# Kernel optimization log

Hardware: AMD Instinct MI355X
Metric: run time of the kernel (lower is better)

## Reference

```python
import jax, jax.numpy as jnp
import numpy as np

Np_, Ny, Nu = 5, 8, 4
NZ = Np_ * (Ny + Nu)  # 60


def setup_inputs() -> dict:
    key = jax.random.key(0)
    ks = jax.random.split(key, 6)
    B, T = 8192, 1024
    u = jax.random.normal(ks[0], (B, T, Nu), dtype=jnp.float32)
    z0 = jax.random.normal(ks[1], (B, NZ), dtype=jnp.float32)
    W1 = jax.random.normal(ks[2], (NZ, 128), dtype=jnp.float32) * (1.0 / np.sqrt(NZ))
    b1 = jnp.zeros((128,), dtype=jnp.float32)
    W2 = jax.random.normal(ks[3], (128, 128), dtype=jnp.float32) * (1.0 / np.sqrt(128))
    b2 = jnp.zeros((128,), dtype=jnp.float32)
    W3 = jax.random.normal(ks[4], (128, Ny), dtype=jnp.float32) * (1.0 / np.sqrt(128))
    b3 = jnp.zeros((Ny,), dtype=jnp.float32)
    return {"u": u, "z0": z0, "W1": W1, "b1": b1, "W2": W2, "b2": b2,
            "W3": W3, "b3": b3}


def reference(u, z0, W1, b1, W2, b2, W3, b3):
    # u: [B, T, Nu], z0: [B, Np*(Ny+Nu)] -> y sequence [B, T, Ny]
    def step(z, u_t):
        h = jnp.tanh(z @ W1 + b1)
        h = jnp.tanh(h @ W2 + b2)
        y = h @ W3 + b3                      # [B, Ny]
        ypseq = z[:, : Np_ * Ny]
        upseq = z[:, Np_ * Ny:]
        z_new = jnp.concatenate(
            (ypseq[:, Ny:], y, upseq[:, Nu:], u_t), axis=-1)
        return z_new, y

    u_tbc = jnp.transpose(u, (1, 0, 2))      # [T, B, Nu]
    _, ys = jax.lax.scan(step, z0, u_tbc)    # ys: [T, B, Ny]
    return jnp.transpose(ys, (1, 0, 2))      # [B, T, Ny]
```

## Files before the change

### kernel.cpp

```cpp
#include <hip/hip_runtime.h>

#define T_STEPS 1024
#define NZV 60
#define H 128
#define NY 8
#define NU 4
#define ZSTR 72
#define HSTR 136

typedef __attribute__((ext_vector_type(8))) short bf16x8;
typedef __attribute__((ext_vector_type(4))) short bf16x4;
typedef __attribute__((ext_vector_type(4))) float f32x4;

__device__ __forceinline__ unsigned short f2bf(float x) {
    unsigned u = __float_as_uint(x);
    u += 0x7FFFu + ((u >> 16) & 1u);
    return (unsigned short)(u >> 16);
}

__device__ __forceinline__ unsigned cvt_pk_bf16(float lo, float hi) {
    unsigned r;
    asm("v_cvt_pk_bf16_f32 %0, %1, %2" : "=v"(r) : "v"(lo), "v"(hi));
    return r;
}

__device__ __forceinline__ float tanh_fast(float x) {
    float e = __builtin_amdgcn_exp2f(x * 2.8853900817779268f);
    return fmaf(-2.0f, __builtin_amdgcn_rcpf(e + 1.0f), 1.0f);
}

__global__ __launch_bounds__(256, 2)
void cstr_scan_kernel(const float* __restrict__ u_g, const float* __restrict__ z0_g,
                      const float* __restrict__ W1, const float* __restrict__ b1,
                      const float* __restrict__ W2, const float* __restrict__ b2,
                      const float* __restrict__ W3, const float* __restrict__ b3,
                      float* __restrict__ out) {
    __shared__ unsigned short zbuf[2][16][ZSTR];
    __shared__ unsigned short h1s[16][HSTR];
    __shared__ unsigned short h2s[16][HSTR];
    __shared__ float ybuf[16][16][NY];

    const int tid   = threadIdx.x;
    const int wid   = tid >> 6;
    const int lane  = tid & 63;
    const int b0    = blockIdx.x * 16;
    const int col   = lane & 15;
    const int kg    = lane >> 4;
    const int wrow0 = kg * 4;
    const int urow  = lane >> 2;
    const int uc    = lane & 3;
    const int nbase = wid * 32;

    bf16x8 w1f[2][2], w2f[4][2], w3f[4];
    float b1v[2], b2v[2], b3v;
#pragma unroll
    for (int nl = 0; nl < 2; ++nl) {
        b1v[nl] = b1[nbase + nl * 16 + col];
        b2v[nl] = b2[nbase + nl * 16 + col];
    }
    b3v = (col < NY) ? b3[col] : 0.f;

#pragma unroll
    for (int kc = 0; kc < 2; ++kc)
#pragma unroll
        for (int nl = 0; nl < 2; ++nl) {
            bf16x8 v;
#pragma unroll
            for (int j = 0; j < 8; ++j) {
                int k = kc * 32 + kg * 8 + j;
                float w = (k < NZV) ? W1[k * H + nbase + nl * 16 + col] : 0.f;
                v[j] = (short)f2bf(w);
            }
            w1f[kc][nl] = v;
        }
#pragma unroll
    for (int kc = 0; kc < 4; ++kc)
#pragma unroll
        for (int nl = 0; nl < 2; ++nl) {
            bf16x8 v;
#pragma unroll
            for (int j = 0; j < 8; ++j) {
                int k = kc * 32 + kg * 8 + j;
                v[j] = (short)f2bf(W2[k * H + nbase + nl * 16 + col]);
            }
            w2f[kc][nl] = v;
        }
#pragma unroll
    for (int kc = 0; kc < 4; ++kc) {
        bf16x8 v;
#pragma unroll
        for (int j = 0; j < 8; ++j) {
            int k = kc * 32 + kg * 8 + j;
            float w = (col < NY) ? W3[k * NY + col] : 0.f;
            v[j] = (short)f2bf(w);
        }
        w3f[kc] = v;
    }

    {
        unsigned short* zs = &zbuf[0][0][0];
        for (int i = tid; i < 2 * 16 * ZSTR; i += 256) zs[i] = 0;
        __syncthreads();
        for (int i = tid; i < 16 * NZV; i += 256) {
            int r = i / NZV, c = i - r * NZV;
            zbuf[0][r][c] = f2bf(z0_g[(size_t)(b0 + r) * NZV + c]);
        }
        __syncthreads();
    }

    const float* uptr = u_g + (size_t)(b0 + urow) * (T_STEPS * NU) + uc;
    float ureg = 0.f, ureg_n = 0.f;
    if (wid == 3) ureg = *uptr;

    int t = 0;

#define STEP_BODY(CUR)                                                                  \
    {                                                                                   \
        const int nxt = (CUR) ^ 1;                                                      \
                                    \
        bf16x8 za0 = *(const bf16x8*)&zbuf[CUR][col][kg * 8];                           \
        bf16x8 za1 = *(const bf16x8*)&zbuf[CUR][col][32 + kg * 8];                      \
        _Pragma("unroll")                                                               \
        for (int nl = 0; nl < 2; ++nl) {                                                \
            f32x4 c1 = { b1v[nl], b1v[nl], b1v[nl], b1v[nl] };                          \
            c1 = __builtin_amdgcn_mfma_f32_16x16x32_bf16(za0, w1f[0][nl], c1, 0, 0, 0); \
            c1 = __builtin_amdgcn_mfma_f32_16x16x32_bf16(za1, w1f[1][nl], c1, 0, 0, 0); \
            unsigned p01 = cvt_pk_bf16(tanh_fast(c1[0]), tanh_fast(c1[1]));             \
            unsigned p23 = cvt_pk_bf16(tanh_fast(c1[2]), tanh_fast(c1[3]));             \
            const int n = nbase + nl * 16 + col;                                        \
            h1s[wrow0 + 0][n] = (unsigned short)p01;                                    \
            h1s[wrow0 + 1][n] = (unsigned short)(p01 >> 16);                            \
            h1s[wrow0 + 2][n] = (unsigned short)p23;                                    \
            h1s[wrow0 + 3][n] = (unsigned short)(p23 >> 16);                            \
        }                                                                               \
                \
        if (wid == 3) {                                                                 \
            bf16x4 m0 = *(const bf16x4*)&zbuf[CUR][urow][8 + 8 * uc];                   \
            bf16x4 m1 = *(const bf16x4*)&zbuf[CUR][urow][12 + 8 * uc];                  \
            bf16x4 m2 = *(const bf16x4*)&zbuf[CUR][urow][44 + 4 * uc];                  \
            *(bf16x4*)&zbuf[nxt][urow][8 * uc]      = m0;                               \
            *(bf16x4*)&zbuf[nxt][urow][8 * uc + 4]  = m1;                               \
            *(bf16x4*)&zbuf[nxt][urow][40 + 4 * uc] = m2;                               \
            zbuf[nxt][urow][56 + uc] = f2bf(ureg);                                      \
            uptr += NU;                                                                 \
            if (t + 1 < T_STEPS) ureg_n = *uptr;                                        \
        }                                                                               \
        __syncthreads();                      \
                                              \
        bf16x8 ha0 = *(const bf16x8*)&h1s[col][0 * 32 + kg * 8];                        \
        bf16x8 ha1 = *(const bf16x8*)&h1s[col][1 * 32 + kg * 8];                        \
        bf16x8 ha2 = *(const bf16x8*)&h1s[col][2 * 32 + kg * 8];                        \
        bf16x8 ha3 = *(const bf16x8*)&h1s[col][3 * 32 + kg * 8];                        \
        _Pragma("unroll")                                                               \
        for (int nl = 0; nl < 2; ++nl) {                                                \
            f32x4 a0 = { b2v[nl], b2v[nl], b2v[nl], b2v[nl] };                          \
            f32x4 a1 = { 0.f, 0.f, 0.f, 0.f };                                          \
            a0 = __builtin_amdgcn_mfma_f32_16x16x32_bf16(ha0, w2f[0][nl], a0, 0, 0, 0); \
            a1 = __builtin_amdgcn_mfma_f32_16x16x32_bf16(ha1, w2f[1][nl], a1, 0, 0, 0); \
            a0 = __builtin_amdgcn_mfma_f32_16x16x32_bf16(ha2, w2f[2][nl], a0, 0, 0, 0); \
            a1 = __builtin_amdgcn_mfma_f32_16x16x32_bf16(ha3, w2f[3][nl], a1, 0, 0, 0); \
            f32x4 c2 = a0 + a1;                                                         \
            unsigned p01 = cvt_pk_bf16(tanh_fast(c2[0]), tanh_fast(c2[1]));             \
            unsigned p23 = cvt_pk_bf16(tanh_fast(c2[2]), tanh_fast(c2[3]));             \
            const int n = nbase + nl * 16 + col;                                        \
            h2s[wrow0 + 0][n] = (unsigned short)p01;                                    \
            h2s[wrow0 + 1][n] = (unsigned short)(p01 >> 16);                            \
            h2s[wrow0 + 2][n] = (unsigned short)p23;                                    \
            h2s[wrow0 + 3][n] = (unsigned short)(p23 >> 16);                            \
        }                                                                               \
        __syncthreads();                                              \
                              \
        if (wid == 0) {                                                                 \
            bf16x8 hp0 = *(const bf16x8*)&h2s[col][0 * 32 + kg * 8];                    \
            bf16x8 hp1 = *(const bf16x8*)&h2s[col][1 * 32 + kg * 8];                    \
            bf16x8 hp2 = *(const bf16x8*)&h2s[col][2 * 32 + kg * 8];                    \
            bf16x8 hp3 = *(const bf16x8*)&h2s[col][3 * 32 + kg * 8];                    \
            f32x4 ya = { b3v, b3v, b3v, b3v };                                          \
            f32x4 yb = { 0.f, 0.f, 0.f, 0.f };                                          \
            ya = __builtin_amdgcn_mfma_f32_16x16x32_bf16(hp0, w3f[0], ya, 0, 0, 0);     \
            yb = __builtin_amdgcn_mfma_f32_16x16x32_bf16(hp1, w3f[1], yb, 0, 0, 0);     \
            ya = __builtin_amdgcn_mfma_f32_16x16x32_bf16(hp2, w3f[2], ya, 0, 0, 0);     \
            yb = __builtin_amdgcn_mfma_f32_16x16x32_bf16(hp3, w3f[3], yb, 0, 0, 0);     \
            f32x4 y = ya + yb;                                                          \
            if (col < NY) {                                                             \
                unsigned q01 = cvt_pk_bf16(y[0], y[1]);                                 \
                unsigned q23 = cvt_pk_bf16(y[2], y[3]);                                 \
                zbuf[nxt][wrow0 + 0][32 + col] = (unsigned short)q01;                   \
                zbuf[nxt][wrow0 + 1][32 + col] = (unsigned short)(q01 >> 16);           \
                zbuf[nxt][wrow0 + 2][32 + col] = (unsigned short)q23;                   \
                zbuf[nxt][wrow0 + 3][32 + col] = (unsigned short)(q23 >> 16);           \
                const int ts = t & 15;                                                  \
                ybuf[ts][wrow0 + 0][col] = y[0];                                        \
                ybuf[ts][wrow0 + 1][col] = y[1];                                        \
                ybuf[ts][wrow0 + 2][col] = y[2];                                        \
                ybuf[ts][wrow0 + 3][col] = y[3];                                        \
            }                                                                           \
        }                                                                               \
        __syncthreads();               \
        ureg = ureg_n;                                                                  \
        ++t;                                                                            \
    }

    const int frow  = tid >> 4;
    const int ftoff = tid & 15;

#define FLUSH(BASE_T)                                                                   \
    {                                                                                   \
        const f32x4* yp = (const f32x4*)&ybuf[ftoff][frow][0];                          \
        f32x4 v0 = yp[0], v1 = yp[1];                                                   \
        float* op = out + ((size_t)(b0 + frow) * T_STEPS + (BASE_T) + ftoff) * NY;      \
        *(f32x4*)op = v0;                                                               \
        *(f32x4*)(op + 4) = v1;                                                         \
    }

#pragma unroll 1
    for (int it = 0; it < T_STEPS / 2; ++it) {
        if ((t & 15) == 0 && t > 0)
            FLUSH(t - 16);
        STEP_BODY(0)
        STEP_BODY(1)
    }
    FLUSH(T_STEPS - 16);
#undef STEP_BODY
#undef FLUSH
}

extern "C" void kernel_launch(void* const* d_in, const int* in_sizes, int n_in,
                              void* d_out, int out_size, void* d_ws, size_t ws_size,
                              hipStream_t stream) {
    (void)in_sizes; (void)n_in; (void)d_ws; (void)ws_size; (void)out_size;
    const float* u  = (const float*)d_in[0];
    const float* z0 = (const float*)d_in[1];
    const float* W1 = (const float*)d_in[2];
    const float* b1 = (const float*)d_in[3];
    const float* W2 = (const float*)d_in[4];
    const float* b2 = (const float*)d_in[5];
    const float* W3 = (const float*)d_in[6];
    const float* b3 = (const float*)d_in[7];
    float* out = (float*)d_out;

    dim3 grid(8192 / 16);
    dim3 block(256);
    cstr_scan_kernel<<<grid, block, 0, stream>>>(u, z0, W1, b1, W2, b2, W3, b3, out);
}
```

Before: 1.083 ms.

## Fuse layer-3 output into next step's layer-1 to drop a barrier per step

Every wave now redundantly computes the small W3 output (with transposed operands) at the start of the next step. The fresh y values are fed straight into the layer-1 A operand through a lane shuffle instead of waiting for a shared-memory round trip. This removes the third __syncthreads per timestep and the serialized single-wave layer-3 phase, at the cost of extra MFMAs on all four waves. The change also double-buffers h2s and ybuf to avoid races, and adds a prologue and epilogue for the pipeline.

```diff
diff --git a/kernel.cpp b/kernel.cpp
--- a/kernel.cpp
+++ b/kernel.cpp
@@ -12,6 +12,8 @@
 typedef __attribute__((ext_vector_type(4))) short bf16x4;
 typedef __attribute__((ext_vector_type(4))) float f32x4;
 
+union U4 { unsigned u[4]; bf16x8 v; };
+
 __device__ __forceinline__ unsigned short f2bf(float x) {
     unsigned u = __float_as_uint(x);
     u += 0x7FFFu + ((u >> 16) & 1u);
@@ -28,6 +30,8 @@
     float e = __builtin_amdgcn_exp2f(x * 2.8853900817779268f);
     return fmaf(-2.0f, __builtin_amdgcn_rcpf(e + 1.0f), 1.0f);
 }
+
+#define MFMA __builtin_amdgcn_mfma_f32_16x16x32_bf16
 
 __global__ __launch_bounds__(256, 2)
 void cstr_scan_kernel(const float* __restrict__ u_g, const float* __restrict__ z0_g,
@@ -37,8 +41,8 @@
                       float* __restrict__ out) {
     __shared__ unsigned short zbuf[2][16][ZSTR];
     __shared__ unsigned short h1s[16][HSTR];
-    __shared__ unsigned short h2s[16][HSTR];
-    __shared__ float ybuf[16][16][NY];
+    __shared__ unsigned short h2s[2][16][HSTR];
+    __shared__ float ybuf[32][16][NY];
 
     const int tid   = threadIdx.x;
     const int wid   = tid >> 6;
@@ -50,16 +54,22 @@
     const int urow  = lane >> 2;
     const int uc    = lane & 3;
     const int nbase = wid * 32;
-
-    bf16x8 w1f[2][2], w2f[4][2], w3f[4];
-    float b1v[2], b2v[2], b3v;
+    const int frow  = tid >> 4;
+    const int ftoff = tid & 15;
+
+    bf16x8 w1f[2][2], w2f[4][2], w3tf[4];
+    float b1v[2], b2v[2];
+    f32x4 b3t;
 #pragma unroll
     for (int nl = 0; nl < 2; ++nl) {
         b1v[nl] = b1[nbase + nl * 16 + col];
         b2v[nl] = b2[nbase + nl * 16 + col];
     }
-    b3v = (col < NY) ? b3[col] : 0.f;
-
+#pragma unroll
+    for (int r = 0; r < 4; ++r) {
+        int m = kg * 4 + r;
+        b3t[r] = (m < NY) ? b3[m] : 0.f;
+    }
 #pragma unroll
     for (int kc = 0; kc < 2; ++kc)
 #pragma unroll
@@ -94,7 +104,7 @@
             float w = (col < NY) ? W3[k * NY + col] : 0.f;
             v[j] = (short)f2bf(w);
         }
-        w3f[kc] = v;
+        w3tf[kc] = v;
     }
 
     {
@@ -112,19 +122,92 @@
     float ureg = 0.f, ureg_n = 0.f;
     if (wid == 3) ureg = *uptr;
 
-    int t = 0;
-
-#define STEP_BODY(CUR)                                                                  \
+    {
+        bf16x8 za0 = *(const bf16x8*)&zbuf[0][col][kg * 8];
+        bf16x8 za1 = *(const bf16x8*)&zbuf[0][col][32 + kg * 8];
+#pragma unroll
+        for (int nl = 0; nl < 2; ++nl) {
+            f32x4 c1 = { b1v[nl], b1v[nl], b1v[nl], b1v[nl] };
+            c1 = MFMA(za0, w1f[0][nl], c1, 0, 0, 0);
+            c1 = MFMA(za1, w1f[1][nl], c1, 0, 0, 0);
+            unsigned p01 = cvt_pk_bf16(tanh_fast(c1[0]), tanh_fast(c1[1]));
+            unsigned p23 = cvt_pk_bf16(tanh_fast(c1[2]), tanh_fast(c1[3]));
+            const int n = nbase + nl * 16 + col;
+            h1s[wrow0 + 0][n] = (unsigned short)p01;
+            h1s[wrow0 + 1][n] = (unsigned short)(p01 >> 16);
+            h1s[wrow0 + 2][n] = (unsigned short)p23;
+            h1s[wrow0 + 3][n] = (unsigned short)(p23 >> 16);
+        }
+        if (wid == 3) {
+            bf16x4 m0 = *(const bf16x4*)&zbuf[0][urow][8 + 8 * uc];
+            bf16x4 m1 = *(const bf16x4*)&zbuf[0][urow][12 + 8 * uc];
+            bf16x4 m2 = *(const bf16x4*)&zbuf[0][urow][44 + 4 * uc];
+            *(bf16x4*)&zbuf[1][urow][8 * uc]      = m0;
+            *(bf16x4*)&zbuf[1][urow][8 * uc + 4]  = m1;
+            *(bf16x4*)&zbuf[1][urow][40 + 4 * uc] = m2;
+            zbuf[1][urow][56 + uc] = f2bf(ureg);
+            uptr += NU;
+            ureg_n = *uptr;
+        }
+        __syncthreads();
+        bf16x8 ha0 = *(const bf16x8*)&h1s[col][0 * 32 + kg * 8];
+        bf16x8 ha1 = *(const bf16x8*)&h1s[col][1 * 32 + kg * 8];
+        bf16x8 ha2 = *(const bf16x8*)&h1s[col][2 * 32 + kg * 8];
+        bf16x8 ha3 = *(const bf16x8*)&h1s[col][3 * 32 + kg * 8];
+#pragma unroll
+        for (int nl = 0; nl < 2; ++nl) {
+            f32x4 a0 = { b2v[nl], b2v[nl], b2v[nl], b2v[nl] };
+            f32x4 a1 = { 0.f, 0.f, 0.f, 0.f };
+            a0 = MFMA(ha0, w2f[0][nl], a0, 0, 0, 0);
+            a1 = MFMA(ha1, w2f[1][nl], a1, 0, 0, 0);
+            a0 = MFMA(ha2, w2f[2][nl], a0, 0, 0, 0);
+            a1 = MFMA(ha3, w2f[3][nl], a1, 0, 0, 0);
+            f32x4 c2 = a0 + a1;
+            unsigned p01 = cvt_pk_bf16(tanh_fast(c2[0]), tanh_fast(c2[1]));
+            unsigned p23 = cvt_pk_bf16(tanh_fast(c2[2]), tanh_fast(c2[3]));
+            const int n = nbase + nl * 16 + col;
+            h2s[1][wrow0 + 0][n] = (unsigned short)p01;
+            h2s[1][wrow0 + 1][n] = (unsigned short)(p01 >> 16);
+            h2s[1][wrow0 + 2][n] = (unsigned short)p23;
+            h2s[1][wrow0 + 3][n] = (unsigned short)(p23 >> 16);
+        }
+        __syncthreads();
+        ureg = ureg_n;
+    }
+
+    int t = 1;
+
+#define BODY(P)                                                                         \
     {                                                                                   \
-        const int nxt = (CUR) ^ 1;                                                      \
-                                    \
-        bf16x8 za0 = *(const bf16x8*)&zbuf[CUR][col][kg * 8];                           \
-        bf16x8 za1 = *(const bf16x8*)&zbuf[CUR][col][32 + kg * 8];                      \
+        bf16x8 hp0 = *(const bf16x8*)&h2s[P][col][0 * 32 + kg * 8];                     \
+        bf16x8 hp1 = *(const bf16x8*)&h2s[P][col][1 * 32 + kg * 8];                     \
+        bf16x8 hp2 = *(const bf16x8*)&h2s[P][col][2 * 32 + kg * 8];                     \
+        bf16x8 hp3 = *(const bf16x8*)&h2s[P][col][3 * 32 + kg * 8];                     \
+        bf16x8 za0  = *(const bf16x8*)&zbuf[P][col][kg * 8];                            \
+        bf16x8 za1l = *(const bf16x8*)&zbuf[P][col][32 + kg * 8];                       \
+        f32x4 ya = b3t;                                                                 \
+        f32x4 yb = { 0.f, 0.f, 0.f, 0.f };                                              \
+        ya = MFMA(w3tf[0], hp0, ya, 0, 0, 0);                                           \
+        yb = MFMA(w3tf[1], hp1, yb, 0, 0, 0);                                           \
+        ya = MFMA(w3tf[2], hp2, ya, 0, 0, 0);                                           \
+        yb = MFMA(w3tf[3], hp3, yb, 0, 0, 0);                                           \
+        f32x4 yv = ya + yb;               \
+        unsigned d0 = cvt_pk_bf16(yv[0], yv[1]);                                        \
+        unsigned d1 = cvt_pk_bf16(yv[2], yv[3]);                                        \
+        unsigned o0 = (unsigned)__shfl((int)d0, col + 16);                              \
+        unsigned o1 = (unsigned)__shfl((int)d1, col + 16);                              \
+        U4 zb_; zb_.u[0] = d0; zb_.u[1] = d1; zb_.u[2] = o0; zb_.u[3] = o1;             \
+        bf16x8 za1 = (kg == 0) ? zb_.v : za1l;      \
+        if (wid == 0 && kg < 2) {                                                       \
+            *(f32x4*)&ybuf[(t - 1) & 31][col][kg * 4] = yv;                             \
+            unsigned* zp = (unsigned*)&zbuf[P ^ 1][col][24 + kg * 4];                   \
+            zp[0] = d0; zp[1] = d1;                  \
+        }                                                                               \
         _Pragma("unroll")                                                               \
         for (int nl = 0; nl < 2; ++nl) {                                                \
             f32x4 c1 = { b1v[nl], b1v[nl], b1v[nl], b1v[nl] };                          \
-            c1 = __builtin_amdgcn_mfma_f32_16x16x32_bf16(za0, w1f[0][nl], c1, 0, 0, 0); \
-            c1 = __builtin_amdgcn_mfma_f32_16x16x32_bf16(za1, w1f[1][nl], c1, 0, 0, 0); \
+            c1 = MFMA(za0, w1f[0][nl], c1, 0, 0, 0);                                    \
+            c1 = MFMA(za1, w1f[1][nl], c1, 0, 0, 0);                                    \
             unsigned p01 = cvt_pk_bf16(tanh_fast(c1[0]), tanh_fast(c1[1]));             \
             unsigned p23 = cvt_pk_bf16(tanh_fast(c1[2]), tanh_fast(c1[3]));             \
             const int n = nbase + nl * 16 + col;                                        \
@@ -133,20 +216,20 @@
             h1s[wrow0 + 2][n] = (unsigned short)p23;                                    \
             h1s[wrow0 + 3][n] = (unsigned short)(p23 >> 16);                            \
         }                                                                               \
-                \
-        if (wid == 3) {                                                                 \
-            bf16x4 m0 = *(const bf16x4*)&zbuf[CUR][urow][8 + 8 * uc];                   \
-            bf16x4 m1 = *(const bf16x4*)&zbuf[CUR][urow][12 + 8 * uc];                  \
-            bf16x4 m2 = *(const bf16x4*)&zbuf[CUR][urow][44 + 4 * uc];                  \
-            *(bf16x4*)&zbuf[nxt][urow][8 * uc]      = m0;                               \
-            *(bf16x4*)&zbuf[nxt][urow][8 * uc + 4]  = m1;                               \
-            *(bf16x4*)&zbuf[nxt][urow][40 + 4 * uc] = m2;                               \
-            zbuf[nxt][urow][56 + uc] = f2bf(ureg);                                      \
+        if (wid == 3) {     \
+            if (uc < 3) {                                                               \
+                bf16x4 m0 = *(const bf16x4*)&zbuf[P][urow][8 + 8 * uc];                 \
+                bf16x4 m1 = *(const bf16x4*)&zbuf[P][urow][12 + 8 * uc];                \
+                *(bf16x4*)&zbuf[P ^ 1][urow][8 * uc]     = m0;                          \
+                *(bf16x4*)&zbuf[P ^ 1][urow][8 * uc + 4] = m1;                          \
+            }                                                                           \
+            bf16x4 m2 = *(const bf16x4*)&zbuf[P][urow][44 + 4 * uc];                    \
+            *(bf16x4*)&zbuf[P ^ 1][urow][40 + 4 * uc] = m2;                             \
+            zbuf[P ^ 1][urow][56 + uc] = f2bf(ureg);                                    \
             uptr += NU;                                                                 \
             if (t + 1 < T_STEPS) ureg_n = *uptr;                                        \
         }                                                                               \
-        __syncthreads();                      \
-                                              \
+        __syncthreads();                                                        \
         bf16x8 ha0 = *(const bf16x8*)&h1s[col][0 * 32 + kg * 8];                        \
         bf16x8 ha1 = *(const bf16x8*)&h1s[col][1 * 32 + kg * 8];                        \
         bf16x8 ha2 = *(const bf16x8*)&h1s[col][2 * 32 + kg * 8];                        \
@@ -155,74 +238,61 @@
         for (int nl = 0; nl < 2; ++nl) {                                                \
             f32x4 a0 = { b2v[nl], b2v[nl], b2v[nl], b2v[nl] };                          \
             f32x4 a1 = { 0.f, 0.f, 0.f, 0.f };                                          \
-            a0 = __builtin_amdgcn_mfma_f32_16x16x32_bf16(ha0, w2f[0][nl], a0, 0, 0, 0); \
-            a1 = __builtin_amdgcn_mfma_f32_16x16x32_bf16(ha1, w2f[1][nl], a1, 0, 0, 0); \
-            a0 = __builtin_amdgcn_mfma_f32_16x16x32_bf16(ha2, w2f[2][nl], a0, 0, 0, 0); \
-            a1 = __builtin_amdgcn_mfma_f32_16x16x32_bf16(ha3, w2f[3][nl], a1, 0, 0, 0); \
+            a0 = MFMA(ha0, w2f[0][nl], a0, 0, 0, 0);                                    \
+            a1 = MFMA(ha1, w2f[1][nl], a1, 0, 0, 0);                                    \
+            a0 = MFMA(ha2, w2f[2][nl], a0, 0, 0, 0);                                    \
+            a1 = MFMA(ha3, w2f[3][nl], a1, 0, 0, 0);                                    \
             f32x4 c2 = a0 + a1;                                                         \
             unsigned p01 = cvt_pk_bf16(tanh_fast(c2[0]), tanh_fast(c2[1]));             \
             unsigned p23 = cvt_pk_bf16(tanh_fast(c2[2]), tanh_fast(c2[3]));             \
             const int n = nbase + nl * 16 + col;                                        \
-            h2s[wrow0 + 0][n] = (unsigned short)p01;                                    \
-            h2s[wrow0 + 1][n] = (unsigned short)(p01 >> 16);                            \
-            h2s[wrow0 + 2][n] = (unsigned short)p23;                                    \
-            h2s[wrow0 + 3][n] = (unsigned short)(p23 >> 16);                            \
+            h2s[P ^ 1][wrow0 + 0][n] = (unsigned short)p01;                             \
+            h2s[P ^ 1][wrow0 + 1][n] = (unsigned short)(p01 >> 16);                     \
+            h2s[P ^ 1][wrow0 + 2][n] = (unsigned short)p23;                             \
+            h2s[P ^ 1][wrow0 + 3][n] = (unsigned short)(p23 >> 16);                     \
         }                                                                               \
-        __syncthreads();                                              \
-                              \
-        if (wid == 0) {                                                                 \
-            bf16x8 hp0 = *(const bf16x8*)&h2s[col][0 * 32 + kg * 8];                    \
-            bf16x8 hp1 = *(const bf16x8*)&h2s[col][1 * 32 + kg * 8];                    \
-            bf16x8 hp2 = *(const bf16x8*)&h2s[col][2 * 32 + kg * 8];                    \
-            bf16x8 hp3 = *(const bf16x8*)&h2s[col][3 * 32 + kg * 8];                    \
-            f32x4 ya = { b3v, b3v, b3v, b3v };                                          \
-            f32x4 yb = { 0.f, 0.f, 0.f, 0.f };                                          \
-            ya = __builtin_amdgcn_mfma_f32_16x16x32_bf16(hp0, w3f[0], ya, 0, 0, 0);     \
-            yb = __builtin_amdgcn_mfma_f32_16x16x32_bf16(hp1, w3f[1], yb, 0, 0, 0);     \
-            ya = __builtin_amdgcn_mfma_f32_16x16x32_bf16(hp2, w3f[2], ya, 0, 0, 0);     \
-            yb = __builtin_amdgcn_mfma_f32_16x16x32_bf16(hp3, w3f[3], yb, 0, 0, 0);     \
-            f32x4 y = ya + yb;                                                          \
-            if (col < NY) {                                                             \
-                unsigned q01 = cvt_pk_bf16(y[0], y[1]);                                 \
-                unsigned q23 = cvt_pk_bf16(y[2], y[3]);                                 \
-                zbuf[nxt][wrow0 + 0][32 + col] = (unsigned short)q01;                   \
-                zbuf[nxt][wrow0 + 1][32 + col] = (unsigned short)(q01 >> 16);           \
-                zbuf[nxt][wrow0 + 2][32 + col] = (unsigned short)q23;                   \
-                zbuf[nxt][wrow0 + 3][32 + col] = (unsigned short)(q23 >> 16);           \
-                const int ts = t & 15;                                                  \
-                ybuf[ts][wrow0 + 0][col] = y[0];                                        \
-                ybuf[ts][wrow0 + 1][col] = y[1];                                        \
-                ybuf[ts][wrow0 + 2][col] = y[2];                                        \
-                ybuf[ts][wrow0 + 3][col] = y[3];                                        \
-            }                                                                           \
-        }                                                                               \
-        __syncthreads();               \
+        __syncthreads();                                                        \
         ureg = ureg_n;                                                                  \
         ++t;                                                                            \
     }
 
-    const int frow  = tid >> 4;
-    const int ftoff = tid & 15;
-
-#define FLUSH(BASE_T)                                                                   \
-    {                                                                                   \
-        const f32x4* yp = (const f32x4*)&ybuf[ftoff][frow][0];                          \
-        f32x4 v0 = yp[0], v1 = yp[1];                                                   \
-        float* op = out + ((size_t)(b0 + frow) * T_STEPS + (BASE_T) + ftoff) * NY;      \
-        *(f32x4*)op = v0;                                                               \
-        *(f32x4*)(op + 4) = v1;                                                         \
-    }
-
 #pragma unroll 1
-    for (int it = 0; it < T_STEPS / 2; ++it) {
-        if ((t & 15) == 0 && t > 0)
-            FLUSH(t - 16);
-        STEP_BODY(0)
-        STEP_BODY(1)
-    }
-    FLUSH(T_STEPS - 16);
-#undef STEP_BODY
-#undef FLUSH
+    for (int it = 0; it < 511; ++it) {
+        if ((t & 15) == 1 && t > 1) {
+            const int bt = t - 17;
+            const f32x4* yp = (const f32x4*)&ybuf[(bt & 31) + ftoff][frow][0];
+            f32x4 v0 = yp[0], v1 = yp[1];
+            float* op = out + ((size_t)(b0 + frow) * T_STEPS + bt + ftoff) * NY;
+            *(f32x4*)op = v0;
+            *(f32x4*)(op + 4) = v1;
+        }
+        BODY(1)
+        BODY(0)
+    }
+    BODY(1)
+#undef BODY
+
+    {
+        bf16x8 hp0 = *(const bf16x8*)&h2s[0][col][0 * 32 + kg * 8];
+        bf16x8 hp1 = *(const bf16x8*)&h2s[0][col][1 * 32 + kg * 8];
+        bf16x8 hp2 = *(const bf16x8*)&h2s[0][col][2 * 32 + kg * 8];
+        bf16x8 hp3 = *(const bf16x8*)&h2s[0][col][3 * 32 + kg * 8];
+        f32x4 ya = b3t;
+        f32x4 yb = { 0.f, 0.f, 0.f, 0.f };
+        ya = MFMA(w3tf[0], hp0, ya, 0, 0, 0);
+        yb = MFMA(w3tf[1], hp1, yb, 0, 0, 0);
+        ya = MFMA(w3tf[2], hp2, ya, 0, 0, 0);
+        yb = MFMA(w3tf[3], hp3, yb, 0, 0, 0);
+        f32x4 yv = ya + yb;
+        if (wid == 0 && kg < 2)
+            *(f32x4*)&ybuf[31][col][kg * 4] = yv;
+        __syncthreads();
+        const f32x4* yp = (const f32x4*)&ybuf[16 + ftoff][frow][0];
+        f32x4 v0 = yp[0], v1 = yp[1];
+        float* op = out + ((size_t)(b0 + frow) * T_STEPS + 1008 + ftoff) * NY;
+        *(f32x4*)op = v0;
+        *(f32x4*)(op + 4) = v1;
+    }
 }
 
 extern "C" void kernel_launch(void* const* d_in, const int* in_sizes, int n_in,
```

Result: slower. 1.111 ms (+2.6%).

## Prefetch u windows into LDS via global_load_lds and hoist z fragment loads

Applied to the files above, without the earlier changes.

Replaces the per-step scalar global load of u by wave 3 with double-buffered 16-step windows that wave 1 loads asynchronously straight into LDS through global_load_lds, one window ahead. This takes a global-memory latency off the serial per-step critical path. It also moves the za0/za1 LDS reads to the end of the previous step, right after the barrier, so they overlap with the loop overhead. The risk is correctness: wave 3 reads ubuf with no explicit vmcnt wait for the async LDS writes, relying on the barrier and 16 steps of lead time, and the window index mapping must match the lds layout.

```diff
diff --git a/kernel.cpp b/kernel.cpp
--- a/kernel.cpp
+++ b/kernel.cpp
@@ -39,6 +39,7 @@
     __shared__ unsigned short h1s[16][HSTR];
     __shared__ unsigned short h2s[16][HSTR];
     __shared__ float ybuf[16][16][NY];
+    __shared__ float ubuf[2][16][16][NU];
 
     const int tid   = threadIdx.x;
     const int wid   = tid >> 6;
@@ -97,6 +98,18 @@
         w3f[kc] = v;
     }
 
+#define LOAD_UWIN(BI, T0)                                                              \
+    if (wid == 1) {                                                                    \
+        const float* usrc = u_g + (size_t)(b0 + (lane & 15)) * (T_STEPS * NU)          \
+                            + (size_t)((T0) + (lane >> 4)) * NU;                       \
+        _Pragma("unroll")                                                              \
+        for (int k_ = 0; k_ < 4; ++k_)                                                 \
+            __builtin_amdgcn_global_load_lds(                                          \
+                (const __attribute__((address_space(1))) unsigned*)(usrc + k_ * 16),   \
+                (__attribute__((address_space(3))) unsigned*)(&ubuf[BI][k_ * 4][0][0]),\
+                16, 0, 0);                                                             \
+    }
+
     {
         unsigned short* zs = &zbuf[0][0][0];
         for (int i = tid; i < 2 * 16 * ZSTR; i += 256) zs[i] = 0;
@@ -105,21 +118,19 @@
             int r = i / NZV, c = i - r * NZV;
             zbuf[0][r][c] = f2bf(z0_g[(size_t)(b0 + r) * NZV + c]);
         }
+        LOAD_UWIN(0, 0)
         __syncthreads();
     }
 
-    const float* uptr = u_g + (size_t)(b0 + urow) * (T_STEPS * NU) + uc;
-    float ureg = 0.f, ureg_n = 0.f;
-    if (wid == 3) ureg = *uptr;
-
     int t = 0;
+
+    bf16x8 za0 = *(const bf16x8*)&zbuf[0][col][kg * 8];
+    bf16x8 za1 = *(const bf16x8*)&zbuf[0][col][32 + kg * 8];
 
 #define STEP_BODY(CUR)                                                                  \
     {                                                                                   \
         const int nxt = (CUR) ^ 1;                                                      \
-                                    \
-        bf16x8 za0 = *(const bf16x8*)&zbuf[CUR][col][kg * 8];                           \
-        bf16x8 za1 = *(const bf16x8*)&zbuf[CUR][col][32 + kg * 8];                      \
+                    \
         _Pragma("unroll")                                                               \
         for (int nl = 0; nl < 2; ++nl) {                                                \
             f32x4 c1 = { b1v[nl], b1v[nl], b1v[nl], b1v[nl] };                          \
@@ -133,7 +144,7 @@
             h1s[wrow0 + 2][n] = (unsigned short)p23;                                    \
             h1s[wrow0 + 3][n] = (unsigned short)(p23 >> 16);                            \
         }                                                                               \
-                \
+             \
         if (wid == 3) {                                                                 \
             bf16x4 m0 = *(const bf16x4*)&zbuf[CUR][urow][8 + 8 * uc];                   \
             bf16x4 m1 = *(const bf16x4*)&zbuf[CUR][urow][12 + 8 * uc];                  \
@@ -141,9 +152,8 @@
             *(bf16x4*)&zbuf[nxt][urow][8 * uc]      = m0;                               \
             *(bf16x4*)&zbuf[nxt][urow][8 * uc + 4]  = m1;                               \
             *(bf16x4*)&zbuf[nxt][urow][40 + 4 * uc] = m2;                               \
-            zbuf[nxt][urow][56 + uc] = f2bf(ureg);                                      \
-            uptr += NU;                                                                 \
-            if (t + 1 < T_STEPS) ureg_n = *uptr;                                        \
+            float uv = ubuf[(t >> 4) & 1][t & 15][urow][uc];                            \
+            zbuf[nxt][urow][56 + uc] = f2bf(uv);                                        \
         }                                                                               \
         __syncthreads();                      \
                                               \
@@ -197,7 +207,9 @@
             }                                                                           \
         }                                                                               \
         __syncthreads();               \
-        ureg = ureg_n;                                                                  \
+                                      \
+        za0 = *(const bf16x8*)&zbuf[nxt][col][kg * 8];                                  \
+        za1 = *(const bf16x8*)&zbuf[nxt][col][32 + kg * 8];                             \
         ++t;                                                                            \
     }
 
@@ -215,14 +227,19 @@
 
 #pragma unroll 1
     for (int it = 0; it < T_STEPS / 2; ++it) {
-        if ((t & 15) == 0 && t > 0)
-            FLUSH(t - 16);
+        if ((t & 15) == 0) {
+            if (t > 0)
+                FLUSH(t - 16);
+            if (t + 16 < T_STEPS)
+                LOAD_UWIN(((t >> 4) & 1) ^ 1, t + 16)
+        }
         STEP_BODY(0)
         STEP_BODY(1)
     }
     FLUSH(T_STEPS - 16);
 #undef STEP_BODY
 #undef FLUSH
+#undef LOAD_UWIN
 }
 
 extern "C" void kernel_launch(void* const* d_in, const int* in_sizes, int n_in,
```

Measured after the change: 1.084 ms. No clear change (+0.1%).
